# Kernel optimization log

Hardware: AMD Instinct MI355X
Metric: run time of the kernel (lower is better)

## Reference

```python
import jax, jax.numpy as jnp
import numpy as np

B = 4096
N_PATCH = 196  # (28/2)^2


def _rx(theta):
    # theta [...] -> RX matrix [..., 2, 2] complex64
    c = jnp.cos(theta / 2) + 0j
    s = -1j * jnp.sin(theta / 2)
    return jnp.stack([jnp.stack([c, s], -1), jnp.stack([s, c], -1)], -2).astype(jnp.complex64)


def _rot(phi, theta, omega):
    # PennyLane Rot(phi, theta, omega) = RZ(omega) RY(theta) RZ(phi), returns [2,2] complex64
    ct = jnp.cos(theta / 2)
    st = jnp.sin(theta / 2)
    m00 = jnp.exp(-1j * (phi + omega) / 2) * ct
    m01 = -jnp.exp(1j * (phi - omega) / 2) * st
    m10 = jnp.exp(-1j * (phi - omega) / 2) * st
    m11 = jnp.exp(1j * (phi + omega) / 2) * ct
    return jnp.stack([jnp.stack([m00, m01]), jnp.stack([m10, m11])]).astype(jnp.complex64)


def _apply_shared(state, U, w):
    # state [N,2,2,2,2], U [2,2] shared across batch, acting on wire w
    s = jnp.moveaxis(state, 1 + w, -1)
    s = jnp.einsum('...a,ba->...b', s, U)
    return jnp.moveaxis(s, -1, 1 + w)


def _apply_batched(state, U, w):
    # U [N,2,2] per-sample gate
    s = jnp.moveaxis(state, 1 + w, -1)
    s = jnp.einsum('n...a,nba->n...b', s, U)
    return jnp.moveaxis(s, -1, 1 + w)


def _cnot(state, c, t):
    s = jnp.moveaxis(state, (1 + c, 1 + t), (-2, -1))
    s = jnp.stack([s[..., 0, :], s[..., 1, ::-1]], axis=-2)
    return jnp.moveaxis(s, (-2, -1), (1 + c, 1 + t))


def _quanv(patches, wq):
    # patches [N,4] angles; wq [n_app, n_layers, 4, 3]
    N = patches.shape[0]
    state = jnp.zeros((N, 16), jnp.complex64).at[:, 0].set(1.0).reshape(N, 2, 2, 2, 2)
    for w in range(4):  # AngleEmbedding: RX per wire
        state = _apply_batched(state, _rx(patches[:, w]), w)
    ranges = (1, 2)  # SEL default: (l % (n_wires-1)) + 1
    for app in range(wq.shape[0]):
        for l in range(wq.shape[1]):
            for w in range(4):
                state = _apply_shared(state, _rot(wq[app, l, w, 0], wq[app, l, w, 1], wq[app, l, w, 2]), w)
            r = ranges[l]
            for w in range(4):
                state = _cnot(state, w, (w + r) % 4)
    p = jnp.abs(state) ** 2  # [N,2,2,2,2]
    feats = []
    for w in range(4):  # <Z_w> = P(bit_w=0) - P(bit_w=1)
        axes = tuple(a for a in range(1, 5) if a != 1 + w)
        m = p.sum(axes)
        feats.append(m[:, 0] - m[:, 1])
    return jnp.stack(feats, -1)  # [N,4]


def _qfc(params, wfc):
    # 1-qubit circuit: RX embedding then Rot gates only (SEL has no entanglers on 1 wire)
    Bq = params.shape[0]
    state = jnp.zeros((Bq, 2), jnp.complex64).at[:, 0].set(1.0)
    state = jnp.einsum('na,nba->nb', state, _rx(params[:, 0]))
    for app in range(wfc.shape[0]):
        for l in range(wfc.shape[1]):
            U = _rot(wfc[app, l, 0, 0], wfc[app, l, 0, 1], wfc[app, l, 0, 2])
            state = jnp.einsum('na,ba->nb', state, U)
    p = jnp.abs(state) ** 2
    return p[:, 0] - p[:, 1]  # [B]


def setup_inputs() -> dict:
    key = jax.random.key(0)
    k1, k2, k3, k4 = jax.random.split(key, 4)
    return {
        'x': jax.random.normal(k1, (B, 784), jnp.float32),
        'weights_q': jax.random.normal(k2, (2, 2, 4, 3), jnp.float32),
        'weights_fc': jax.random.normal(k3, (3, 3, 1, 3), jnp.float32),
        'W_out': jax.random.normal(k4, (10, 1), jnp.float32) * 0.1,
        'b_out': jnp.zeros((10,), jnp.float32),
    }


def reference(x, weights_q, weights_fc, W_out, b_out):
    Bb = x.shape[0]
    img = x.reshape(Bb, 28, 28)
    # extract 2x2 stride-2 patches in (row-block, col-block) order, row-major within patch
    patches = img.reshape(Bb, 14, 2, 14, 2).transpose(0, 1, 3, 2, 4).reshape(Bb * N_PATCH, 4)
    feats = _quanv(patches, weights_q).reshape(Bb, N_PATCH * 4)  # [B,784]
    q = _qfc(feats[:, :1], weights_fc)  # [B]
    logits = q[:, None] @ W_out.T + b_out  # Linear(1,10) -> [B,10]
    return jax.nn.log_softmax(logits, axis=-1)
```

## Files before the change

### kernel.cpp

```cpp
#include <hip/hip_runtime.h>
#include <math.h>


struct c32 { float re, im; };

__device__ __forceinline__ c32 cmul(c32 a, c32 b) {
    return { fmaf(a.re, b.re, -a.im * b.im), fmaf(a.re, b.im, a.im * b.re) };
}
__device__ __forceinline__ c32 cmulc(c32 a, c32 b) {
    return { fmaf(a.re, b.re, a.im * b.im), fmaf(a.re, b.im, -a.im * b.re) };
}
__device__ __forceinline__ c32 cadd(c32 a, c32 b) { return { a.re + b.re, a.im + b.im }; }
__device__ __forceinline__ c32 csub(c32 a, c32 b) { return { a.re - b.re, a.im - b.im }; }

template<int W>
__device__ __forceinline__ void apply1(c32 amp[16], c32 u00, c32 u01, c32 u10, c32 u11) {
    constexpr int s = 8 >> W;
    #pragma unroll
    for (int i = 0; i < 16; ++i) {
        if (i & s) continue;
        c32 a = amp[i], b = amp[i + s];
        amp[i]     = cadd(cmul(u00, a), cmul(u01, b));
        amp[i + s] = cadd(cmul(u10, a), cmul(u11, b));
    }
}

template<int C, int T>
__device__ __forceinline__ void cnot4(c32 amp[16]) {
    constexpr int sc = 8 >> C, st = 8 >> T;
    #pragma unroll
    for (int i = 0; i < 16; ++i) {
        if ((i & sc) && !(i & st)) {
            c32 tmp = amp[i]; amp[i] = amp[i | st]; amp[i | st] = tmp;
        }
    }
}

__device__ __forceinline__ void make_rot(float phi, float th, float om,
                                         c32& u00, c32& u01, c32& u10, c32& u11) {
    float sh, ch; sincosf(th * 0.5f, &sh, &ch);
    float spo, cpo; sincosf((phi + om) * 0.5f, &spo, &cpo);
    float spm, cpm; sincosf((phi - om) * 0.5f, &spm, &cpm);
    u00 = {  cpo * ch, -spo * ch };
    u01 = { -cpm * sh, -spm * sh };
    u10 = {  cpm * sh, -spm * sh };
    u11 = {  cpo * ch,  spo * ch };
}

#define GP 20

__global__ __launch_bounds__(256)
void quanv_hybrid_kernel(const float* __restrict__ x,
                         const float* __restrict__ wq,
                         const float* __restrict__ wfc,
                         const float* __restrict__ Wout,
                         const float* __restrict__ bout,
                         float* __restrict__ out,
                         int B)
{
    const int tid = threadIdx.x;
    const int j   = tid & 15;
    const int img = blockIdx.x * 16 + (tid >> 4);
    const int imgc = (img < B) ? img : (B - 1);

    __shared__ c32   gmat[25][4];
    __shared__ float Ur[16][16], Ui[16][16];
    __shared__ float Gqs[16 * GP];
    __shared__ float yz[2];

    const float* xb = x + (size_t)imgc * 784;
    float2 a01 = *reinterpret_cast<const float2*>(xb);
    float2 a23 = *reinterpret_cast<const float2*>(xb + 28);
    float Wj = (j < 10) ? Wout[j] : 0.f;
    float bj = (j < 10) ? bout[j] : 0.f;

    if (tid < 25) {
        const float* p = (tid < 16) ? (wq + 3 * tid) : (wfc + 3 * (tid - 16));
        c32 a, bb, c, d;
        make_rot(p[0], p[1], p[2], a, bb, c, d);
        gmat[tid][0] = a; gmat[tid][1] = bb; gmat[tid][2] = c; gmat[tid][3] = d;
    }
    __syncthreads();

    if (tid < 16) {
        c32 amp[16];
        #pragma unroll
        for (int i = 0; i < 16; ++i) amp[i] = { 0.f, 0.f };
        amp[tid].re = 1.f;

        #pragma unroll
        for (int al = 0; al < 4; ++al) {
            apply1<0>(amp, gmat[al*4+0][0], gmat[al*4+0][1], gmat[al*4+0][2], gmat[al*4+0][3]);
            apply1<1>(amp, gmat[al*4+1][0], gmat[al*4+1][1], gmat[al*4+1][2], gmat[al*4+1][3]);
            apply1<2>(amp, gmat[al*4+2][0], gmat[al*4+2][1], gmat[al*4+2][2], gmat[al*4+2][3]);
            apply1<3>(amp, gmat[al*4+3][0], gmat[al*4+3][1], gmat[al*4+3][2], gmat[al*4+3][3]);
            if ((al & 1) == 0) {
                cnot4<0,1>(amp); cnot4<1,2>(amp); cnot4<2,3>(amp); cnot4<3,0>(amp);
            } else {
                cnot4<0,2>(amp); cnot4<1,3>(amp); cnot4<2,0>(amp); cnot4<3,1>(amp);
            }
        }
        #pragma unroll
        for (int i = 0; i < 16; ++i) { Ur[i][tid] = amp[i].re; Ui[i][tid] = amp[i].im; }
    } else if (tid == 16) {
        c32 v00 = {1.f, 0.f}, v01 = {0.f, 0.f}, v10 = {0.f, 0.f}, v11 = {1.f, 0.f};
        #pragma unroll
        for (int g = 0; g < 9; ++g) {
            c32 u00 = gmat[16+g][0], u01 = gmat[16+g][1], u10 = gmat[16+g][2], u11 = gmat[16+g][3];
            c32 n00 = cadd(cmul(u00, v00), cmul(u01, v10));
            c32 n01 = cadd(cmul(u00, v01), cmul(u01, v11));
            c32 n10 = cadd(cmul(u10, v00), cmul(u11, v10));
            c32 n11 = cadd(cmul(u10, v01), cmul(u11, v11));
            v00 = n00; v01 = n01; v10 = n10; v11 = n11;
        }
        float zH = fmaf(v00.re, v00.re, v00.im * v00.im)
                 - fmaf(v10.re, v10.re, v10.im * v10.im);
        c32 h01 = csub(cmulc(v00, v01), cmulc(v10, v11));
        yz[0] = -h01.im; yz[1] = zH;
    }
    __syncthreads();

    {
        int jj = tid >> 4, kk = tid & 15;
        float mre = 0.f, mim = 0.f;
        #pragma unroll
        for (int i = 0; i < 16; ++i) {
            float ar = Ur[i][jj], ai = Ui[i][jj], br = Ur[i][kk], bi = Ui[i][kk];
            float re = fmaf(ar, br,  ai * bi);
            float im = fmaf(ar, bi, -ai * br);
            if (i < 8) { mre += re; mim += im; } else { mre -= re; mim -= im; }
        }
        int m4 = (__popc(jj) - __popc(kk)) & 3;
        float g = (m4 == 0) ? mre : (m4 == 1) ? -mim : (m4 == 2) ? -mre : mim;
        Gqs[jj * GP + kk] = g;
    }
    __syncthreads();

    float s0, c0, s1, c1, s2, c2, s3, c3;
    sincosf(a01.x * 0.5f, &s0, &c0);
    sincosf(a01.y * 0.5f, &s1, &c1);
    sincosf(a23.x * 0.5f, &s2, &c2);
    sincosf(a23.y * 0.5f, &s3, &c3);

    float A[4]  = { c0 * c1, c0 * s1, s0 * c1, s0 * s1 };
    float Bv[4] = { c2 * c3, c2 * s3, s2 * c3, s2 * s3 };
    float r[16];
    #pragma unroll
    for (int k = 0; k < 16; ++k) r[k] = A[k >> 2] * Bv[k & 3];

    const float* gr = &Gqs[j * GP];
    float4 g0 = *reinterpret_cast<const float4*>(gr + 0);
    float4 g1 = *reinterpret_cast<const float4*>(gr + 4);
    float4 g2 = *reinterpret_cast<const float4*>(gr + 8);
    float4 g3 = *reinterpret_cast<const float4*>(gr + 12);
    float t = 0.f;
    t = fmaf(g0.x, r[0],  t); t = fmaf(g0.y, r[1],  t);
    t = fmaf(g0.z, r[2],  t); t = fmaf(g0.w, r[3],  t);
    t = fmaf(g1.x, r[4],  t); t = fmaf(g1.y, r[5],  t);
    t = fmaf(g1.z, r[6],  t); t = fmaf(g1.w, r[7],  t);
    t = fmaf(g2.x, r[8],  t); t = fmaf(g2.y, r[9],  t);
    t = fmaf(g2.z, r[10], t); t = fmaf(g2.w, r[11], t);
    t = fmaf(g3.x, r[12], t); t = fmaf(g3.y, r[13], t);
    t = fmaf(g3.z, r[14], t); t = fmaf(g3.w, r[15], t);

    float z0 = r[j] * t;
    z0 += __shfl_xor(z0, 1);
    z0 += __shfl_xor(z0, 2);
    z0 += __shfl_xor(z0, 4);
    z0 += __shfl_xor(z0, 8);

    float sz, cz; sincosf(z0, &sz, &cz);
    float q = fmaf(cz, yz[1], -sz * yz[0]);

    float lg = (j < 10) ? fmaf(q, Wj, bj) : -1e30f;
    float m = lg;
    m = fmaxf(m, __shfl_xor(m, 1));
    m = fmaxf(m, __shfl_xor(m, 2));
    m = fmaxf(m, __shfl_xor(m, 4));
    m = fmaxf(m, __shfl_xor(m, 8));

    float e = (j < 10) ? expf(lg - m) : 0.f;
    float sum = e;
    sum += __shfl_xor(sum, 1);
    sum += __shfl_xor(sum, 2);
    sum += __shfl_xor(sum, 4);
    sum += __shfl_xor(sum, 8);

    float lse = m + logf(sum);
    if (j < 10 && img < B) out[(size_t)img * 10 + j] = lg - lse;
}

extern "C" void kernel_launch(void* const* d_in, const int* in_sizes, int n_in,
                              void* d_out, int out_size, void* d_ws, size_t ws_size,
                              hipStream_t stream) {
    const float* x    = (const float*)d_in[0];
    const float* wq   = (const float*)d_in[1];
    const float* wfc  = (const float*)d_in[2];
    const float* Wout = (const float*)d_in[3];
    const float* bout = (const float*)d_in[4];
    float* out = (float*)d_out;

    int B = in_sizes[0] / 784;
    int blocks = (B + 15) / 16;
    quanv_hybrid_kernel<<<blocks, 256, 0, stream>>>(x, wq, wfc, Wout, bout, out, B);
}
```

Baseline: 74.88 us.

## Split 16-gate circuit unitary build across two lanes and combine via matmul

Measured after the change: 74.90 us. Within noise of the previous version (+0.0%).

```diff
diff --git a/kernel.cpp b/kernel.cpp
--- a/kernel.cpp
+++ b/kernel.cpp
@@ -45,6 +45,19 @@
     u01 = { -cpm * sh, -spm * sh };
     u10 = {  cpm * sh, -spm * sh };
     u11 = {  cpo * ch,  spo * ch };
+}
+
+__device__ __forceinline__ void sim_app(c32 amp[16], const c32 (*gm)[4], int base) {
+    apply1<0>(amp, gm[base+0][0], gm[base+0][1], gm[base+0][2], gm[base+0][3]);
+    apply1<1>(amp, gm[base+1][0], gm[base+1][1], gm[base+1][2], gm[base+1][3]);
+    apply1<2>(amp, gm[base+2][0], gm[base+2][1], gm[base+2][2], gm[base+2][3]);
+    apply1<3>(amp, gm[base+3][0], gm[base+3][1], gm[base+3][2], gm[base+3][3]);
+    cnot4<0,1>(amp); cnot4<1,2>(amp); cnot4<2,3>(amp); cnot4<3,0>(amp);
+    apply1<0>(amp, gm[base+4][0], gm[base+4][1], gm[base+4][2], gm[base+4][3]);
+    apply1<1>(amp, gm[base+5][0], gm[base+5][1], gm[base+5][2], gm[base+5][3]);
+    apply1<2>(amp, gm[base+6][0], gm[base+6][1], gm[base+6][2], gm[base+6][3]);
+    apply1<3>(amp, gm[base+7][0], gm[base+7][1], gm[base+7][2], gm[base+7][3]);
+    cnot4<0,2>(amp); cnot4<1,3>(amp); cnot4<2,0>(amp); cnot4<3,1>(amp);
 }
 
 #define GP 20
@@ -64,6 +77,8 @@
     const int imgc = (img < B) ? img : (B - 1);
 
     __shared__ c32   gmat[25][4];
+    __shared__ float Ar[16][16], Ai[16][16];
+    __shared__ float Br_[16][16], Bi_[16][16];
     __shared__ float Ur[16][16], Ui[16][16];
     __shared__ float Gqs[16 * GP];
     __shared__ float yz[2];
@@ -82,27 +97,22 @@
     }
     __syncthreads();
 
-    if (tid < 16) {
+    if (tid < 32) {
+        const int t = tid & 15;
         c32 amp[16];
         #pragma unroll
         for (int i = 0; i < 16; ++i) amp[i] = { 0.f, 0.f };
-        amp[tid].re = 1.f;
-
-        #pragma unroll
-        for (int al = 0; al < 4; ++al) {
-            apply1<0>(amp, gmat[al*4+0][0], gmat[al*4+0][1], gmat[al*4+0][2], gmat[al*4+0][3]);
-            apply1<1>(amp, gmat[al*4+1][0], gmat[al*4+1][1], gmat[al*4+1][2], gmat[al*4+1][3]);
-            apply1<2>(amp, gmat[al*4+2][0], gmat[al*4+2][1], gmat[al*4+2][2], gmat[al*4+2][3]);
-            apply1<3>(amp, gmat[al*4+3][0], gmat[al*4+3][1], gmat[al*4+3][2], gmat[al*4+3][3]);
-            if ((al & 1) == 0) {
-                cnot4<0,1>(amp); cnot4<1,2>(amp); cnot4<2,3>(amp); cnot4<3,0>(amp);
-            } else {
-                cnot4<0,2>(amp); cnot4<1,3>(amp); cnot4<2,0>(amp); cnot4<3,1>(amp);
-            }
-        }
-        #pragma unroll
-        for (int i = 0; i < 16; ++i) { Ur[i][tid] = amp[i].re; Ui[i][tid] = amp[i].im; }
-    } else if (tid == 16) {
+        amp[t].re = 1.f;
+        if (tid < 16) {
+            sim_app(amp, gmat, 0);
+            #pragma unroll
+            for (int i = 0; i < 16; ++i) { Ar[i][t] = amp[i].re; Ai[i][t] = amp[i].im; }
+        } else {
+            sim_app(amp, gmat, 8);
+            #pragma unroll
+            for (int i = 0; i < 16; ++i) { Br_[i][t] = amp[i].re; Bi_[i][t] = amp[i].im; }
+        }
+    } else if (tid == 32) {
         c32 v00 = {1.f, 0.f}, v01 = {0.f, 0.f}, v10 = {0.f, 0.f}, v11 = {1.f, 0.f};
         #pragma unroll
         for (int g = 0; g < 9; ++g) {
@@ -121,7 +131,20 @@
     __syncthreads();
 
     {
-        int jj = tid >> 4, kk = tid & 15;
+        const int i = tid >> 4, t = tid & 15;
+        c32 acc = { 0.f, 0.f };
+        #pragma unroll
+        for (int k = 0; k < 16; ++k) {
+            c32 bk = { Br_[i][k], Bi_[i][k] };
+            c32 ak = { Ar[k][t],  Ai[k][t]  };
+            acc = cadd(acc, cmul(bk, ak));
+        }
+        Ur[i][t] = acc.re; Ui[i][t] = acc.im;
+    }
+    __syncthreads();
+
+    {
+        const int jj = tid >> 4, kk = tid & 15;
         float mre = 0.f, mim = 0.f;
         #pragma unroll
         for (int i = 0; i < 16; ++i) {
@@ -142,11 +165,11 @@
     sincosf(a23.x * 0.5f, &s2, &c2);
     sincosf(a23.y * 0.5f, &s3, &c3);
 
-    float A[4]  = { c0 * c1, c0 * s1, s0 * c1, s0 * s1 };
+    float A4[4] = { c0 * c1, c0 * s1, s0 * c1, s0 * s1 };
     float Bv[4] = { c2 * c3, c2 * s3, s2 * c3, s2 * s3 };
     float r[16];
     #pragma unroll
-    for (int k = 0; k < 16; ++k) r[k] = A[k >> 2] * Bv[k & 3];
+    for (int k = 0; k < 16; ++k) r[k] = A4[k >> 2] * Bv[k & 3];
 
     const float* gr = &Gqs[j * GP];
     float4 g0 = *reinterpret_cast<const float4*>(gr + 0);
```
